# Performance work log

Measured on AMD Instinct MI355X. Metric: run time of the kernel, lower is better.

## Reference

```python
import jax, jax.numpy as jnp
import numpy as np

EMB_SIZE = 768
BLOCK_SIZE = 64
NUM_CLASS = 97
N = 4096
NUM_BLOCKS = EMB_SIZE // BLOCK_SIZE  # 12


def setup_inputs() -> dict:
    key = jax.random.key(0)
    k1, k2, k3 = jax.random.split(key, 3)
    head_embeddings = jax.random.normal(k1, (N, EMB_SIZE), dtype=jnp.float32)
    tail_embeddings = jax.random.normal(k2, (N, EMB_SIZE), dtype=jnp.float32)
    # xavier_uniform for [NUM_CLASS, EMB_SIZE*BLOCK_SIZE]
    fan_in = EMB_SIZE * BLOCK_SIZE
    fan_out = NUM_CLASS
    bound = float(np.sqrt(6.0 / (fan_in + fan_out)))
    W = jax.random.uniform(k3, (NUM_CLASS, EMB_SIZE * BLOCK_SIZE), dtype=jnp.float32,
                           minval=-bound, maxval=bound)
    b = jnp.full((NUM_CLASS,), 0.1, dtype=jnp.float32)
    return {"head_embeddings": head_embeddings, "tail_embeddings": tail_embeddings,
            "W": W, "b": b}


def reference(head_embeddings, tail_embeddings, W, b):
    n = head_embeddings.shape[0]
    b1 = head_embeddings.reshape(n, NUM_BLOCKS, BLOCK_SIZE)  # [N, K, S]
    b2 = tail_embeddings.reshape(n, NUM_BLOCKS, BLOCK_SIZE)  # [N, K, S]
    # block-wise outer product: [N, K, S, S] -> [N, K*S*S]
    bl = jnp.einsum('nki,nkj->nkij', b1, b2).reshape(n, EMB_SIZE * BLOCK_SIZE)
    logits = bl @ W.T + b  # [N, NUM_CLASS]
    return logits
```

## Files before the change

### kernel.cpp

```cpp
#include <hip/hip_runtime.h>
#include <hip/hip_bf16.h>
#include <stdint.h>

#define NROWS 4096
#define NCLS  97
#define EMB   768
#define KTOT  49152
#define OUT_ELEMS (NROWS * NCLS)
#define E_ELEMS  (NROWS * EMB)
#define NK32  (KTOT / 32)
#define WT_BYTES ((size_t)NK32 * 128 * 64)

typedef __attribute__((ext_vector_type(4)))  float floatx4;
typedef _Float16 f16x2 __attribute__((ext_vector_type(2)));
typedef _Float16 f16x8 __attribute__((ext_vector_type(8)));

__device__ __forceinline__ uint4 cvt8h(float4 a, float4 b) {
  f16x8 v;
  v[0] = (_Float16)a.x; v[1] = (_Float16)a.y; v[2] = (_Float16)a.z; v[3] = (_Float16)a.w;
  v[4] = (_Float16)b.x; v[5] = (_Float16)b.y; v[6] = (_Float16)b.z; v[7] = (_Float16)b.w;
  return __builtin_bit_cast(uint4, v);
}

__global__ void prep(const float* __restrict__ W, uint4* __restrict__ wt)
{
  const int nwt = NK32 * 128 * 4;
  int t = blockIdx.x * blockDim.x + threadIdx.x;
  if (t >= nwt) return;
  int eo = t & 3;
  int c  = (t >> 2) & 127;
  int kc = t >> 9;
  uint4 v = uint4{0u, 0u, 0u, 0u};
  if (c < NCLS) {
    const float4* p = (const float4*)(W + (size_t)c * KTOT + kc * 32 + eo * 8);
    v = cvt8h(p[0], p[1]);
  }
  wt[t] = v;
}

__global__ __launch_bounds__(256, 2)
void bilinear_main(const float* __restrict__ b1f,
                   const float* __restrict__ b2f,
                   const char* __restrict__ Wt,
                   const float* __restrict__ biasg,
                   float* __restrict__ P,
                   float* __restrict__ outd,
                   int klen)
{
  const int tid  = threadIdx.x;
  const int w    = tid >> 6;
  const int l    = tid & 63;
  const int l15  = l & 15;
  const int quad = l >> 4;
  const int mhalf = w & 1;
  const int chalf = w >> 1;
  const bool cfull = (chalf == 0);
  const int bm = blockIdx.y;
  const int k0 = blockIdx.x * klen;

  int nrow[4];
#pragma unroll
  for (int rt = 0; rt < 4; ++rt) nrow[rt] = bm * 128 + mhalf * 64 + rt * 16 + l15;

  const char* wtl = Wt + (size_t)(k0 >> 5) * 8192
                       + (chalf * 64 + l15) * 64 + quad * 16;

  floatx4 acc[4][4];
#pragma unroll
  for (int rt = 0; rt < 4; ++rt)
#pragma unroll
    for (int ct = 0; ct < 4; ++ct)
      acc[rt][ct] = floatx4{0.f, 0.f, 0.f, 0.f};

  f16x2 b2h[4][2][4];
  f16x2 sv[4];
  uint4 wfA[2][4], wfB[2][4];

#define LOADWF(buf, iwv)  do {                                              \
    const char* pw_ = wtl + (size_t)(iwv) * 16384;                          \
    _Pragma("unroll")                                                       \
    for (int kh_ = 0; kh_ < 2; ++kh_)                                       \
      _Pragma("unroll")                                                     \
      for (int ct_ = 0; ct_ < 4; ++ct_)                                     \
        if (ct_ < 3 || cfull)                                               \
          buf[kh_][ct_] = *(const uint4*)(pw_ + kh_ * 8192 + ct_ * 1024);   \
  } while (0)

#define COMPUTE(buf)  do {                                                  \
    _Pragma("unroll")                                                       \
    for (int kh_ = 0; kh_ < 2; ++kh_) {                                     \
      _Pragma("unroll")                                                     \
      for (int rt_ = 0; rt_ < 4; ++rt_) {                                   \
        f16x2 p0 = sv[rt_] * b2h[rt_][kh_][0];                              \
        f16x2 p1 = sv[rt_] * b2h[rt_][kh_][1];                              \
        f16x2 p2 = sv[rt_] * b2h[rt_][kh_][2];                              \
        f16x2 p3 = sv[rt_] * b2h[rt_][kh_][3];                              \
        uint4 au;                                                           \
        au.x = __builtin_bit_cast(uint32_t, p0);                            \
        au.y = __builtin_bit_cast(uint32_t, p1);                            \
        au.z = __builtin_bit_cast(uint32_t, p2);                            \
        au.w = __builtin_bit_cast(uint32_t, p3);                            \
        f16x8 af = __builtin_bit_cast(f16x8, au);                           \
        _Pragma("unroll")                                                   \
        for (int ct_ = 0; ct_ < 4; ++ct_)                                   \
          if (ct_ < 3 || cfull)                                             \
            acc[rt_][ct_] = __builtin_amdgcn_mfma_f32_16x16x32_f16(         \
                af, __builtin_bit_cast(f16x8, buf[kh_][ct_]),               \
                acc[rt_][ct_], 0, 0, 0);                                    \
      }                                                                     \
    }                                                                       \
  } while (0)

  int cur_k = -1;
  const int nwin = klen >> 6;

  LOADWF(wfA, 0);

  for (int gwin = 0; gwin < nwin; gwin += 8) {
    const int kap0 = k0 + (gwin << 6);
    const int kblk = kap0 >> 12;
    const int i0   = (kap0 >> 6) & 63;
    if (kblk != cur_k) {
      cur_k = kblk;
#pragma unroll
      for (int rt = 0; rt < 4; ++rt)
#pragma unroll
        for (int kh = 0; kh < 2; ++kh) {
          const float* p = b2f + (size_t)nrow[rt] * EMB + kblk * 64 + kh * 32 + quad * 8;
          float4 v0 = ((const float4*)p)[0];
          float4 v1 = ((const float4*)p)[1];
          b2h[rt][kh][0][0] = (_Float16)v0.x; b2h[rt][kh][0][1] = (_Float16)v0.y;
          b2h[rt][kh][1][0] = (_Float16)v0.z; b2h[rt][kh][1][1] = (_Float16)v0.w;
          b2h[rt][kh][2][0] = (_Float16)v1.x; b2h[rt][kh][2][1] = (_Float16)v1.y;
          b2h[rt][kh][3][0] = (_Float16)v1.z; b2h[rt][kh][3][1] = (_Float16)v1.w;
        }
    }

#pragma unroll
    for (int ih = 0; ih < 2; ++ih) {
      float4 b1v[4];
#pragma unroll
      for (int rt = 0; rt < 4; ++rt)
        b1v[rt] = *(const float4*)(b1f + (size_t)nrow[rt] * EMB +
                                   kblk * 64 + i0 + ih * 4);

#pragma unroll
      for (int ii2 = 0; ii2 < 4; ++ii2) {
        const int s  = ih * 4 + ii2;
        const int iw = gwin + s;
        int ipf = iw + 1;
        if (ipf > nwin - 1) ipf = nwin - 1;

#pragma unroll
        for (int rt = 0; rt < 4; ++rt) {
          _Float16 h = (_Float16)((&b1v[rt].x)[ii2]);
          sv[rt][0] = h; sv[rt][1] = h;
        }

        if ((s & 1) == 0) { LOADWF(wfB, ipf); COMPUTE(wfA); }
        else              { LOADWF(wfA, ipf); COMPUTE(wfB); }
      }
    }
  }
#undef LOADWF
#undef COMPUTE

  if (P) {
    float* Pb = P + (size_t)blockIdx.x * OUT_ELEMS;
#pragma unroll
    for (int rt = 0; rt < 4; ++rt)
#pragma unroll
      for (int ct = 0; ct < 4; ++ct) {
        const int c = chalf * 64 + ct * 16 + l15;
        if (c < NCLS) {
#pragma unroll
          for (int r = 0; r < 4; ++r) {
            const int row = bm * 128 + mhalf * 64 + rt * 16 + quad * 4 + r;
            Pb[(size_t)row * NCLS + c] = acc[rt][ct][r];
          }
        }
      }
  } else {
#pragma unroll
    for (int rt = 0; rt < 4; ++rt)
#pragma unroll
      for (int ct = 0; ct < 4; ++ct) {
        const int c = chalf * 64 + ct * 16 + l15;
        if (c < NCLS) {
          const float bv = biasg[c];
#pragma unroll
          for (int r = 0; r < 4; ++r) {
            const int row = bm * 128 + mhalf * 64 + rt * 16 + quad * 4 + r;
            outd[(size_t)row * NCLS + c] = acc[rt][ct][r] + bv;
          }
        }
      }
  }
}

template<int KSC>
__global__ void reduce_bias_t(const float* __restrict__ P,
                              const float* __restrict__ biasg,
                              float* __restrict__ out)
{
  int i = blockIdx.x * blockDim.x + threadIdx.x;
  const int n4 = OUT_ELEMS / 4;
  if (i >= n4) return;
  int c0 = (i * 4) % NCLS;
  int c1 = c0 + 1 == NCLS ? 0 : c0 + 1;
  int c2 = c1 + 1 == NCLS ? 0 : c1 + 1;
  int c3 = c2 + 1 == NCLS ? 0 : c2 + 1;
  float4 s;
  s.x = biasg[c0]; s.y = biasg[c1]; s.z = biasg[c2]; s.w = biasg[c3];
  const float4* P4 = (const float4*)P;
#pragma unroll
  for (int t = 0; t < KSC; ++t) {
    float4 v = P4[(size_t)t * n4 + i];
    s.x += v.x; s.y += v.y; s.z += v.z; s.w += v.w;
  }
  ((float4*)out)[i] = s;
}

static void launch_reduce(int KS, const float* P, const float* bb, float* out,
                          hipStream_t stream) {
  const int nb = (OUT_ELEMS / 4 + 255) / 256;
  switch (KS) {
    case 16: reduce_bias_t<16><<<nb, 256, 0, stream>>>(P, bb, out); break;
    case 12: reduce_bias_t<12><<<nb, 256, 0, stream>>>(P, bb, out); break;
    case 8:  reduce_bias_t<8><<<nb, 256, 0, stream>>>(P, bb, out);  break;
    case 6:  reduce_bias_t<6><<<nb, 256, 0, stream>>>(P, bb, out);  break;
    case 4:  reduce_bias_t<4><<<nb, 256, 0, stream>>>(P, bb, out);  break;
    case 3:  reduce_bias_t<3><<<nb, 256, 0, stream>>>(P, bb, out);  break;
    case 2:  reduce_bias_t<2><<<nb, 256, 0, stream>>>(P, bb, out);  break;
    default: reduce_bias_t<1><<<nb, 256, 0, stream>>>(P, bb, out);  break;
  }
}

extern "C" void kernel_launch(void* const* d_in, const int* in_sizes, int n_in,
                              void* d_out, int out_size, void* d_ws, size_t ws_size,
                              hipStream_t stream) {
  const float* b1f = (const float*)d_in[0];
  const float* b2f = (const float*)d_in[1];
  const float* Wf  = (const float*)d_in[2];
  const float* bbf = (const float*)d_in[3];
  float* out = (float*)d_out;

  const size_t slice = (size_t)OUT_ELEMS * 4;
  static const int cands[] = {16, 12, 8, 6, 4, 3, 2, 1};
  const int NC = 8;

  int KS = 0;
  for (int i = 0; i < NC; ++i)
    if (WT_BYTES + (size_t)cands[i] * slice <= ws_size) { KS = cands[i]; break; }

  uint4* Wt = (uint4*)d_ws;
  const int nwt = NK32 * 128 * 4;

  prep<<<(nwt + 255) / 256, 256, 0, stream>>>(Wf, Wt);

  if (KS > 0) {
    float* P = (float*)((char*)d_ws + WT_BYTES);
    bilinear_main<<<dim3(KS, 32), 256, 0, stream>>>(
        b1f, b2f, (const char*)Wt, bbf, P, nullptr, KTOT / KS);
    launch_reduce(KS, P, bbf, out, stream);
  } else {
    bilinear_main<<<dim3(1, 32), 256, 0, stream>>>(
        b1f, b2f, (const char*)Wt, bbf, nullptr, out, KTOT);
  }
}
```

Measured before the change: 151.9 us.

## Software-pipeline weight and head loads with inline-asm loads and explicit vmcnt waits

Replaces the compiler-scheduled weight-fragment loads with inline-asm global_load_dwordx4 calls. Explicit s_waitcnt vmcnt counts and scheduling barriers now control exactly when each double-buffered fragment must have arrived. The head-embedding scalars are also prefetched one group ahead into alternating register buffers, so their latency overlaps the MFMA work of the current group. The fourth class tile is now loaded unconditionally, relying on the zero padding in the prepared weights. The aim is to stop the compiler inserting conservative full waits and to hide global-load latency. The risk is that the hand-counted waits are fragile and the asm loads are invisible to the compiler's own dependency tracking.

```diff
diff --git a/kernel.cpp b/kernel.cpp
--- a/kernel.cpp
+++ b/kernel.cpp
@@ -21,6 +21,19 @@
   v[4] = (_Float16)b.x; v[5] = (_Float16)b.y; v[6] = (_Float16)b.z; v[7] = (_Float16)b.w;
   return __builtin_bit_cast(uint4, v);
 }
+
+template<int OFF>
+__device__ __forceinline__ uint4 gl16(const char* p) {
+  uint4 d;
+  asm volatile("global_load_dwordx4 %0, %1, off offset:%2"
+               : "=v"(d) : "v"(p), "i"(OFF));
+  return d;
+}
+
+#define WAITVM(N) do {                                                       \
+    asm volatile("s_waitcnt vmcnt(" #N ")" ::: "memory");                    \
+    __builtin_amdgcn_sched_barrier(0);                                       \
+  } while (0)
 
 __global__ void prep(const float* __restrict__ W, uint4* __restrict__ wt)
 {
@@ -73,97 +86,121 @@
       acc[rt][ct] = floatx4{0.f, 0.f, 0.f, 0.f};
 
   f16x2 b2h[4][2][4];
-  f16x2 sv[4];
   uint4 wfA[2][4], wfB[2][4];
-
-#define LOADWF(buf, iwv)  do {                                              \
-    const char* pw_ = wtl + (size_t)(iwv) * 16384;                          \
-    _Pragma("unroll")                                                       \
-    for (int kh_ = 0; kh_ < 2; ++kh_)                                       \
-      _Pragma("unroll")                                                     \
-      for (int ct_ = 0; ct_ < 4; ++ct_)                                     \
-        if (ct_ < 3 || cfull)                                               \
-          buf[kh_][ct_] = *(const uint4*)(pw_ + kh_ * 8192 + ct_ * 1024);   \
-  } while (0)
-
-#define COMPUTE(buf)  do {                                                  \
-    _Pragma("unroll")                                                       \
-    for (int kh_ = 0; kh_ < 2; ++kh_) {                                     \
-      _Pragma("unroll")                                                     \
-      for (int rt_ = 0; rt_ < 4; ++rt_) {                                   \
-        f16x2 p0 = sv[rt_] * b2h[rt_][kh_][0];                              \
-        f16x2 p1 = sv[rt_] * b2h[rt_][kh_][1];                              \
-        f16x2 p2 = sv[rt_] * b2h[rt_][kh_][2];                              \
-        f16x2 p3 = sv[rt_] * b2h[rt_][kh_][3];                              \
-        uint4 au;                                                           \
-        au.x = __builtin_bit_cast(uint32_t, p0);                            \
-        au.y = __builtin_bit_cast(uint32_t, p1);                            \
-        au.z = __builtin_bit_cast(uint32_t, p2);                            \
-        au.w = __builtin_bit_cast(uint32_t, p3);                            \
-        f16x8 af = __builtin_bit_cast(f16x8, au);                           \
-        _Pragma("unroll")                                                   \
-        for (int ct_ = 0; ct_ < 4; ++ct_)                                   \
-          if (ct_ < 3 || cfull)                                             \
-            acc[rt_][ct_] = __builtin_amdgcn_mfma_f32_16x16x32_f16(         \
-                af, __builtin_bit_cast(f16x8, buf[kh_][ct_]),               \
-                acc[rt_][ct_], 0, 0, 0);                                    \
-      }                                                                     \
-    }                                                                       \
-  } while (0)
-
-  int cur_k = -1;
+  uint4 b1X[4], b1Y[4];
+
+#define LOADB2(kbv) do {                                                      \
+    _Pragma("unroll")                                                         \
+    for (int rt_ = 0; rt_ < 4; ++rt_)                                         \
+      _Pragma("unroll")                                                       \
+      for (int kh_ = 0; kh_ < 2; ++kh_) {                                     \
+        const float* p_ = b2f + (size_t)nrow[rt_] * EMB + (kbv) * 64 +        \
+                          kh_ * 32 + quad * 8;                                \
+        float4 v0_ = ((const float4*)p_)[0];                                  \
+        float4 v1_ = ((const float4*)p_)[1];                                  \
+        b2h[rt_][kh_][0][0] = (_Float16)v0_.x; b2h[rt_][kh_][0][1] = (_Float16)v0_.y; \
+        b2h[rt_][kh_][1][0] = (_Float16)v0_.z; b2h[rt_][kh_][1][1] = (_Float16)v0_.w; \
+        b2h[rt_][kh_][2][0] = (_Float16)v1_.x; b2h[rt_][kh_][2][1] = (_Float16)v1_.y; \
+        b2h[rt_][kh_][3][0] = (_Float16)v1_.z; b2h[rt_][kh_][3][1] = (_Float16)v1_.w; \
+      }                                                                       \
+  } while (0)
+
+#define ISSUE_WF(buf, iwv) do {                                               \
+    const char* pw_  = wtl + (size_t)(iwv) * 16384;                           \
+    const char* pw1_ = pw_ + 8192;                                            \
+    buf[0][0] = gl16<0>(pw_);     buf[0][1] = gl16<1024>(pw_);                \
+    buf[0][2] = gl16<2048>(pw_);  buf[0][3] = gl16<3072>(pw_);                \
+    buf[1][0] = gl16<0>(pw1_);    buf[1][1] = gl16<1024>(pw1_);               \
+    buf[1][2] = gl16<2048>(pw1_); buf[1][3] = gl16<3072>(pw1_);               \
+  } while (0)
+
+#define ISSUE_B1(buf, kapv) do {                                              \
+    _Pragma("unroll")                                                         \
+    for (int rt_ = 0; rt_ < 4; ++rt_)                                         \
+      buf[rt_] = gl16<0>((const char*)(b1f + (size_t)nrow[rt_] * EMB +        \
+                         ((kapv) >> 12) * 64 + (((kapv) >> 6) & 63)));        \
+  } while (0)
+
+#define COMPUTE(BUF, BU, S) do {                                              \
+    f16x2 sv_[4];                                                             \
+    _Pragma("unroll")                                                         \
+    for (int rt_ = 0; rt_ < 4; ++rt_) {                                       \
+      float4 bv_ = __builtin_bit_cast(float4, BU[rt_]);                       \
+      _Float16 h_ = (_Float16)((&bv_.x)[S]);                                  \
+      sv_[rt_][0] = h_; sv_[rt_][1] = h_;                                     \
+    }                                                                         \
+    _Pragma("unroll")                                                         \
+    for (int kh_ = 0; kh_ < 2; ++kh_)                                         \
+      _Pragma("unroll")                                                       \
+      for (int rt_ = 0; rt_ < 4; ++rt_) {                                     \
+        f16x2 p0_ = sv_[rt_] * b2h[rt_][kh_][0];                              \
+        f16x2 p1_ = sv_[rt_] * b2h[rt_][kh_][1];                              \
+        f16x2 p2_ = sv_[rt_] * b2h[rt_][kh_][2];                              \
+        f16x2 p3_ = sv_[rt_] * b2h[rt_][kh_][3];                              \
+        uint4 au_;                                                            \
+        au_.x = __builtin_bit_cast(uint32_t, p0_);                            \
+        au_.y = __builtin_bit_cast(uint32_t, p1_);                            \
+        au_.z = __builtin_bit_cast(uint32_t, p2_);                            \
+        au_.w = __builtin_bit_cast(uint32_t, p3_);                            \
+        f16x8 af_ = __builtin_bit_cast(f16x8, au_);                           \
+        _Pragma("unroll")                                                     \
+        for (int ct_ = 0; ct_ < 4; ++ct_)                                     \
+          if (ct_ < 3 || cfull)                                               \
+            acc[rt_][ct_] = __builtin_amdgcn_mfma_f32_16x16x32_f16(           \
+                af_, __builtin_bit_cast(f16x8, BUF[kh_][ct_]),                \
+                acc[rt_][ct_], 0, 0, 0);                                      \
+      }                                                                       \
+  } while (0)
+
+#define GROUP_BODY(gp, BU, BP) do {                                           \
+    const int kap_g_ = k0 + (gp) * 256;                                       \
+    const int kb_ = kap_g_ >> 12;                                             \
+    if (kb_ != cur_kb) { cur_kb = kb_; LOADB2(kb_); }                         \
+    _Pragma("unroll")                                                         \
+    for (int s = 0; s < 4; ++s) {                                             \
+      const int iw_ = (gp) * 4 + s;                                           \
+      if (s == 3) {                                                           \
+        int hg_ = ((gp) + 1 < ngrp) ? (gp) + 1 : (gp);                        \
+        int kap_h_ = k0 + hg_ * 256;                                          \
+        ISSUE_B1(BP, kap_h_);                                                 \
+      }                                                                       \
+      int ipf_ = (iw_ + 1 < nwin) ? iw_ + 1 : nwin - 1;                       \
+      if ((s & 1) == 0) {                                                     \
+        ISSUE_WF(wfB, ipf_);                                                  \
+        WAITVM(8);                                                            \
+        COMPUTE(wfA, BU, s);                                                  \
+      } else if (s == 1) {                                                    \
+        ISSUE_WF(wfA, ipf_);                                                  \
+        WAITVM(8);                                                            \
+        COMPUTE(wfB, BU, s);                                                  \
+      } else {                      \
+        ISSUE_WF(wfA, ipf_);                                                  \
+        WAITVM(12);                                                           \
+        COMPUTE(wfB, BU, s);                                                  \
+      }                                                                       \
+    }                                                                         \
+  } while (0)
+
   const int nwin = klen >> 6;
-
-  LOADWF(wfA, 0);
-
-  for (int gwin = 0; gwin < nwin; gwin += 8) {
-    const int kap0 = k0 + (gwin << 6);
-    const int kblk = kap0 >> 12;
-    const int i0   = (kap0 >> 6) & 63;
-    if (kblk != cur_k) {
-      cur_k = kblk;
-#pragma unroll
-      for (int rt = 0; rt < 4; ++rt)
-#pragma unroll
-        for (int kh = 0; kh < 2; ++kh) {
-          const float* p = b2f + (size_t)nrow[rt] * EMB + kblk * 64 + kh * 32 + quad * 8;
-          float4 v0 = ((const float4*)p)[0];
-          float4 v1 = ((const float4*)p)[1];
-          b2h[rt][kh][0][0] = (_Float16)v0.x; b2h[rt][kh][0][1] = (_Float16)v0.y;
-          b2h[rt][kh][1][0] = (_Float16)v0.z; b2h[rt][kh][1][1] = (_Float16)v0.w;
-          b2h[rt][kh][2][0] = (_Float16)v1.x; b2h[rt][kh][2][1] = (_Float16)v1.y;
-          b2h[rt][kh][3][0] = (_Float16)v1.z; b2h[rt][kh][3][1] = (_Float16)v1.w;
-        }
-    }
-
-#pragma unroll
-    for (int ih = 0; ih < 2; ++ih) {
-      float4 b1v[4];
-#pragma unroll
-      for (int rt = 0; rt < 4; ++rt)
-        b1v[rt] = *(const float4*)(b1f + (size_t)nrow[rt] * EMB +
-                                   kblk * 64 + i0 + ih * 4);
-
-#pragma unroll
-      for (int ii2 = 0; ii2 < 4; ++ii2) {
-        const int s  = ih * 4 + ii2;
-        const int iw = gwin + s;
-        int ipf = iw + 1;
-        if (ipf > nwin - 1) ipf = nwin - 1;
-
-#pragma unroll
-        for (int rt = 0; rt < 4; ++rt) {
-          _Float16 h = (_Float16)((&b1v[rt].x)[ii2]);
-          sv[rt][0] = h; sv[rt][1] = h;
-        }
-
-        if ((s & 1) == 0) { LOADWF(wfB, ipf); COMPUTE(wfA); }
-        else              { LOADWF(wfA, ipf); COMPUTE(wfB); }
-      }
-    }
-  }
-#undef LOADWF
+  const int ngrp = nwin >> 2;
+
+  int cur_kb = k0 >> 12;
+  LOADB2(cur_kb);
+#pragma unroll
+  for (int rt = 0; rt < 4; ++rt)
+    b1X[rt] = *(const uint4*)(b1f + (size_t)nrow[rt] * EMB +
+                              cur_kb * 64 + ((k0 >> 6) & 63));
+  ISSUE_WF(wfA, 0);
+
+  for (int g2 = 0; g2 < ngrp; g2 += 2) {
+    GROUP_BODY(g2,     b1X, b1Y);
+    GROUP_BODY(g2 + 1, b1Y, b1X);
+  }
+#undef GROUP_BODY
 #undef COMPUTE
+#undef ISSUE_B1
+#undef ISSUE_WF
+#undef LOADB2
 
   if (P) {
     float* Pb = P + (size_t)blockIdx.x * OUT_ELEMS;
```

New measurement: 155.5 us. +2.4%, slower.
